# Performance work log

Hardware: AMD Instinct MI355X
Metric: run time of the kernel (lower is better)

## Reference

```python
import jax, jax.numpy as jnp
import numpy as np

INIT_STDEV = 0.01

def setup_inputs() -> dict:
    key = jax.random.key(0)
    k1, k2, k3 = jax.random.split(key, 3)
    B, S, D = 8, 4096, 768
    x = jax.random.normal(k1, (B, S, D), dtype=jnp.float32)
    att_v = jax.random.normal(k2, (D,), dtype=jnp.float32) * INIT_STDEV
    att_W = jax.random.normal(k3, (D, D), dtype=jnp.float32) * INIT_STDEV
    return {"x": x, "att_v": att_v, "att_W": att_W}

def reference(x, att_v, att_W):
    # y = x @ W : [B,S,D]; scores = tanh(y) . v over D : [B,S]
    y = jnp.tanh(jnp.einsum('bsd,de->bse', x, att_W))
    scores = jnp.einsum('bsd,d->bs', y, att_v)
    weights = jax.nn.softmax(scores, axis=-1)            # softmax over sequence
    out = jnp.einsum('bs,bsd->bd', weights, x)           # attsum pool
    return out.astype(jnp.float32)
```

## Files before the change

kernel.cpp:

```cpp
#include <hip/hip_runtime.h>
#include <hip/hip_bf16.h>

constexpr int Bb = 8;
constexpr int Ss = 4096;
constexpr int Dd = 768;
constexpr int Mm = Bb * Ss;

typedef __bf16 bf16x8 __attribute__((ext_vector_type(8)));
typedef __bf16 bf16x4 __attribute__((ext_vector_type(4)));
typedef float f32x4 __attribute__((ext_vector_type(4)));

__device__ __forceinline__ float fast_tanh(float x) {
    return 1.f - 2.f / (__expf(2.f * x) + 1.f);
}

__device__ __forceinline__ void load_lds16(const void* g, void* l) {
    __builtin_amdgcn_global_load_lds(
        (const __attribute__((address_space(1))) unsigned int*)g,
        (__attribute__((address_space(3))) unsigned int*)l, 16, 0, 0);
}

__global__ __launch_bounds__(256) void convWX(const float* __restrict__ W,
                                              __bf16* __restrict__ Wt,
                                              const float* __restrict__ x,
                                              __bf16* __restrict__ xb) {
    const int bid = blockIdx.x;
    if (bid < 576) {
        __shared__ float tile[32][33];
        const int tx = threadIdx.x & 31;
        const int ty = threadIdx.x >> 5;
        const int kb = (bid % 24) * 32;
        const int nb = (bid / 24) * 32;
#pragma unroll
        for (int i = 0; i < 32; i += 8)
            tile[ty + i][tx] = W[(size_t)(kb + ty + i) * Dd + nb + tx];
        __syncthreads();
#pragma unroll
        for (int i = 0; i < 32; i += 8) {
            const int n = nb + ty + i;
            const int txs = (tx & 7) | ((((tx >> 3) & 3) ^ ((n >> 1) & 3)) << 3);
            Wt[(size_t)n * Dd + kb + txs] = (__bf16)tile[tx][ty + i];
        }
    } else {
        const size_t i = ((size_t)(bid - 576) * 256 + threadIdx.x) * 8;
        const int m = (int)(i / Dd);
        const int k = (int)(i % Dd);
        const int sl = (k >> 3) & 3;
        const int dk = (k & ~31) | (((sl ^ ((m >> 1) & 3)) << 3));
        const float4 a = *(const float4*)(x + i);
        const float4 b = *(const float4*)(x + i + 4);
        bf16x8 p;
        p[0] = (__bf16)a.x; p[1] = (__bf16)a.y; p[2] = (__bf16)a.z; p[3] = (__bf16)a.w;
        p[4] = (__bf16)b.x; p[5] = (__bf16)b.y; p[6] = (__bf16)b.z; p[7] = (__bf16)b.w;
        *(bf16x8*)(xb + (size_t)m * Dd + dk) = p;
    }
}

__global__ __launch_bounds__(512, 4) void scores_gemm(
    const __bf16* __restrict__ xb, const __bf16* __restrict__ Wt,
    const float* __restrict__ v, float* __restrict__ scores3) {
    __shared__ __bf16 As[3][128 * 32];
    __shared__ __bf16 Bs[3][256 * 32];
    __shared__ float ssc[8][64];

    const int t = threadIdx.x;
    const int id = blockIdx.x;
    const int ids = ((id & 7) * 96) + (id >> 3);
    const int mb = ids / 3;
    const int nb = ids - mb * 3;
    const int lane = t & 63;
    const int wave = t >> 6;
    const int wm = wave >> 2;
    const int wn = wave & 3;
    const int quad = lane >> 4;
    const int lid = lane & 15;
    const int rslot = ((quad ^ ((lid >> 1) & 3)) * 8);

    const __bf16* axg = xb + (size_t)(mb * 128 + (t >> 2)) * Dd + (t & 3) * 8;
    const int awl = t * 8;

    const __bf16* bgp[2];
    int blp[2];
#pragma unroll
    for (int j = 0; j < 2; ++j) {
        const int flat = j * 8192 + t * 16;
        const int col = flat >> 6;
        bgp[j] = Wt + (size_t)(nb * 256 + col) * Dd + ((flat & 63) >> 1);
        blp[j] = flat >> 1;
    }

    f32x4 acc[4][4];
#pragma unroll
    for (int tm = 0; tm < 4; ++tm)
#pragma unroll
        for (int nt = 0; nt < 4; ++nt) acc[tm][nt] = (f32x4){0.f, 0.f, 0.f, 0.f};

    load_lds16(axg, &As[0][awl]);
#pragma unroll
    for (int j = 0; j < 2; ++j) load_lds16(bgp[j], &Bs[0][blp[j]]);
    load_lds16(axg + 32, &As[1][awl]);
#pragma unroll
    for (int j = 0; j < 2; ++j) load_lds16(bgp[j] + 32, &Bs[1][blp[j]]);

#pragma unroll
    for (int k = 0; k < 24; ++k) {
        if (k == 23) asm volatile("s_waitcnt vmcnt(0)" ::: "memory");
        else         asm volatile("s_waitcnt vmcnt(3)" ::: "memory");
        __builtin_amdgcn_sched_barrier(0);
        __builtin_amdgcn_s_barrier();
        __builtin_amdgcn_sched_barrier(0);

        if (k < 22) {
            load_lds16(axg + (k + 2) * 32, &As[(k + 2) % 3][awl]);
#pragma unroll
            for (int j = 0; j < 2; ++j)
                load_lds16(bgp[j] + (k + 2) * 32, &Bs[(k + 2) % 3][blp[j]]);
        }
        __builtin_amdgcn_sched_barrier(0);

        bf16x8 af[4], bfr[4];
#pragma unroll
        for (int tm = 0; tm < 4; ++tm)
            af[tm] = *(const bf16x8*)(&As[k % 3][(wm * 64 + tm * 16 + lid) * 32 + rslot]);
#pragma unroll
        for (int nt = 0; nt < 4; ++nt)
            bfr[nt] = *(const bf16x8*)(&Bs[k % 3][(wn * 64 + nt * 16 + lid) * 32 + rslot]);

        __builtin_amdgcn_s_setprio(1);
#pragma unroll
        for (int tm = 0; tm < 4; ++tm)
#pragma unroll
            for (int nt = 0; nt < 4; ++nt)
                acc[tm][nt] = __builtin_amdgcn_mfma_f32_16x16x32_bf16(af[tm], bfr[nt], acc[tm][nt], 0, 0, 0);
        __builtin_amdgcn_s_setprio(0);
    }

    float vv[4];
#pragma unroll
    for (int nt = 0; nt < 4; ++nt)
        vv[nt] = v[nb * 256 + wn * 64 + nt * 16 + lid];

#pragma unroll
    for (int tm = 0; tm < 4; ++tm)
#pragma unroll
        for (int r = 0; r < 4; ++r) {
            float s = 0.f;
#pragma unroll
            for (int nt = 0; nt < 4; ++nt) s += vv[nt] * fast_tanh(acc[tm][nt][r]);
            s += __shfl_xor(s, 1);
            s += __shfl_xor(s, 2);
            s += __shfl_xor(s, 4);
            s += __shfl_xor(s, 8);
            if (lid == 0) ssc[wave][tm * 16 + quad * 4 + r] = s;
        }
    __syncthreads();
    if (t < 128) {
        const int wmh = t >> 6;
        const int rl = t & 63;
        float s = 0.f;
#pragma unroll
        for (int ww = 0; ww < 4; ++ww) s += ssc[wmh * 4 + ww][rl];
        scores3[(size_t)nb * Mm + mb * 128 + t] = s;
    }
}

__global__ __launch_bounds__(192) void pool1e(const __bf16* __restrict__ xb,
                                              const float* __restrict__ scores3,
                                              float* __restrict__ partial,
                                              float* __restrict__ esum) {
    const int b = blockIdx.y;
    const int c = blockIdx.x;
    const int t = threadIdx.x;
    __shared__ float we[32];

    if (t < 32) {
        const size_t i = (size_t)b * Ss + c * 32 + t;
        we[t] = __expf(scores3[i] + scores3[Mm + i] + scores3[2 * Mm + i]);
    }
    __syncthreads();

    const int d0 = t * 4;
    const int kc = d0 & ~31;
    const int sl = (d0 >> 3) & 3;
    const int w8 = d0 & 7;
    const int m0 = b * Ss + c * 32;
    const __bf16* base = xb + (size_t)m0 * Dd;

    float4 acc = make_float4(0.f, 0.f, 0.f, 0.f);
#pragma unroll 8
    for (int i = 0; i < 32; ++i) {
        const float ww = we[i];
        const int phys = kc + ((sl ^ (((m0 + i) >> 1) & 3)) << 3) + w8;
        const bf16x4 xv = *(const bf16x4*)(base + (size_t)i * Dd + phys);
        acc.x += ww * (float)xv[0];
        acc.y += ww * (float)xv[1];
        acc.z += ww * (float)xv[2];
        acc.w += ww * (float)xv[3];
    }
    *(float4*)(partial + ((size_t)(b * 128 + c)) * Dd + d0) = acc;
    if (t == 0) {
        float s = 0.f;
#pragma unroll
        for (int i = 0; i < 32; ++i) s += we[i];
        esum[b * 128 + c] = s;
    }
}

__global__ __launch_bounds__(128) void pool2(const float* __restrict__ partial,
                                             const float* __restrict__ esum,
                                             float* __restrict__ out) {
    const int b = blockIdx.y;
    const int t = threadIdx.x;
    const int d = blockIdx.x * 128 + t;

    float es = 0.f;
    if (t < 64) {
        es = esum[b * 128 + t] + esum[b * 128 + 64 + t];
        es += __shfl_xor(es, 1);
        es += __shfl_xor(es, 2);
        es += __shfl_xor(es, 4);
        es += __shfl_xor(es, 8);
        es += __shfl_xor(es, 16);
        es += __shfl_xor(es, 32);
    }
    __shared__ float esT;
    if (t == 0) esT = es;
    __syncthreads();
    const float inv = 1.f / esT;

    float s = 0.f;
#pragma unroll 8
    for (int c = 0; c < 128; ++c) s += partial[((size_t)(b * 128 + c)) * Dd + d];
    out[(size_t)b * Dd + d] = s * inv;
}

extern "C" void kernel_launch(void* const* d_in, const int* in_sizes, int n_in,
                              void* d_out, int out_size, void* d_ws, size_t ws_size,
                              hipStream_t stream) {
    (void)in_sizes; (void)n_in; (void)ws_size; (void)out_size;
    const float* x = (const float*)d_in[0];
    const float* v = (const float*)d_in[1];
    const float* W = (const float*)d_in[2];

    char* ws = (char*)d_ws;
    constexpr size_t OFF_WT = 0;
    constexpr size_t OFF_SC = 1179648;
    constexpr size_t OFF_ES = OFF_SC + 393216;
    constexpr size_t OFF_PA = OFF_ES + 4096;
    constexpr size_t OFF_XB = OFF_PA + 3145728;

    __bf16* Wt     = (__bf16*)(ws + OFF_WT);
    float* scores3 = (float*)(ws + OFF_SC);
    float* esum    = (float*)(ws + OFF_ES);
    float* partial = (float*)(ws + OFF_PA);
    __bf16* xb     = (__bf16*)(ws + OFF_XB);

    convWX<<<dim3(576 + (Mm * Dd) / (256 * 8)), 256, 0, stream>>>(W, Wt, x, xb);
    scores_gemm<<<dim3(3 * Mm / 128), 512, 0, stream>>>(xb, Wt, v, scores3);
    pool1e<<<dim3(128, Bb), 192, 0, stream>>>(xb, scores3, partial, esum);
    pool2<<<dim3(6, Bb), 128, 0, stream>>>(partial, esum, (float*)d_out);
}
```

Before: 219.9 us.

## Shrink GEMM tile to 128x128 with 256 threads and six N-partitions

Changes the scores GEMM block tile from 128x256 (512 threads, 8 waves) to 128x128 (256 threads, 4 waves). The grid doubles, the partial score buffer grows from three to six slices, and the pooling kernel sums six partials. The smaller tile cuts LDS per block and adds more blocks, which may improve occupancy and load balance across CUs. In exchange, x is reloaded from global memory twice as often and more partial scores have to be written and read back.

```diff
diff --git a/kernel.cpp b/kernel.cpp
--- a/kernel.cpp
+++ b/kernel.cpp
@@ -56,37 +56,35 @@
     }
 }
 
-__global__ __launch_bounds__(512, 4) void scores_gemm(
+__global__ __launch_bounds__(256, 3) void scores_gemm(
     const __bf16* __restrict__ xb, const __bf16* __restrict__ Wt,
-    const float* __restrict__ v, float* __restrict__ scores3) {
+    const float* __restrict__ v, float* __restrict__ scores6) {
     __shared__ __bf16 As[3][128 * 32];
-    __shared__ __bf16 Bs[3][256 * 32];
-    __shared__ float ssc[8][64];
+    __shared__ __bf16 Bs[3][128 * 32];
+    __shared__ float ssc[4][64];
 
     const int t = threadIdx.x;
     const int id = blockIdx.x;
-    const int ids = ((id & 7) * 96) + (id >> 3);
-    const int mb = ids / 3;
-    const int nb = ids - mb * 3;
+    const int ids = ((id & 7) * 192) + (id >> 3);
+    const int mb = ids / 6;
+    const int nb = ids - mb * 6;
     const int lane = t & 63;
     const int wave = t >> 6;
-    const int wm = wave >> 2;
-    const int wn = wave & 3;
+    const int wm = wave >> 1;
+    const int wn = wave & 1;
     const int quad = lane >> 4;
     const int lid = lane & 15;
     const int rslot = ((quad ^ ((lid >> 1) & 3)) * 8);
 
-    const __bf16* axg = xb + (size_t)(mb * 128 + (t >> 2)) * Dd + (t & 3) * 8;
-    const int awl = t * 8;
-
+    const __bf16* axg[2];
     const __bf16* bgp[2];
-    int blp[2];
+    int sl_[2];
 #pragma unroll
     for (int j = 0; j < 2; ++j) {
-        const int flat = j * 8192 + t * 16;
-        const int col = flat >> 6;
-        bgp[j] = Wt + (size_t)(nb * 256 + col) * Dd + ((flat & 63) >> 1);
-        blp[j] = flat >> 1;
+        const int row = j * 64 + (t >> 2);
+        axg[j] = xb + (size_t)(mb * 128 + row) * Dd + (t & 3) * 8;
+        bgp[j] = Wt + (size_t)(nb * 128 + row) * Dd + (t & 3) * 8;
+        sl_[j] = j * 2048 + t * 8;
     }
 
     f32x4 acc[4][4];
@@ -95,26 +93,30 @@
 #pragma unroll
         for (int nt = 0; nt < 4; ++nt) acc[tm][nt] = (f32x4){0.f, 0.f, 0.f, 0.f};
 
-    load_lds16(axg, &As[0][awl]);
-#pragma unroll
-    for (int j = 0; j < 2; ++j) load_lds16(bgp[j], &Bs[0][blp[j]]);
-    load_lds16(axg + 32, &As[1][awl]);
-#pragma unroll
-    for (int j = 0; j < 2; ++j) load_lds16(bgp[j] + 32, &Bs[1][blp[j]]);
+#pragma unroll
+    for (int j = 0; j < 2; ++j) load_lds16(axg[j], &As[0][sl_[j]]);
+#pragma unroll
+    for (int j = 0; j < 2; ++j) load_lds16(bgp[j], &Bs[0][sl_[j]]);
+#pragma unroll
+    for (int j = 0; j < 2; ++j) load_lds16(axg[j] + 32, &As[1][sl_[j]]);
+#pragma unroll
+    for (int j = 0; j < 2; ++j) load_lds16(bgp[j] + 32, &Bs[1][sl_[j]]);
 
 #pragma unroll
     for (int k = 0; k < 24; ++k) {
         if (k == 23) asm volatile("s_waitcnt vmcnt(0)" ::: "memory");
-        else         asm volatile("s_waitcnt vmcnt(3)" ::: "memory");
+        else         asm volatile("s_waitcnt vmcnt(4)" ::: "memory");
         __builtin_amdgcn_sched_barrier(0);
         __builtin_amdgcn_s_barrier();
         __builtin_amdgcn_sched_barrier(0);
 
         if (k < 22) {
-            load_lds16(axg + (k + 2) * 32, &As[(k + 2) % 3][awl]);
 #pragma unroll
             for (int j = 0; j < 2; ++j)
-                load_lds16(bgp[j] + (k + 2) * 32, &Bs[(k + 2) % 3][blp[j]]);
+                load_lds16(axg[j] + (k + 2) * 32, &As[(k + 2) % 3][sl_[j]]);
+#pragma unroll
+            for (int j = 0; j < 2; ++j)
+                load_lds16(bgp[j] + (k + 2) * 32, &Bs[(k + 2) % 3][sl_[j]]);
         }
         __builtin_amdgcn_sched_barrier(0);
 
@@ -138,7 +140,7 @@
     float vv[4];
 #pragma unroll
     for (int nt = 0; nt < 4; ++nt)
-        vv[nt] = v[nb * 256 + wn * 64 + nt * 16 + lid];
+        vv[nt] = v[nb * 128 + wn * 64 + nt * 16 + lid];
 
 #pragma unroll
     for (int tm = 0; tm < 4; ++tm)
@@ -157,15 +159,13 @@
     if (t < 128) {
         const int wmh = t >> 6;
         const int rl = t & 63;
-        float s = 0.f;
-#pragma unroll
-        for (int ww = 0; ww < 4; ++ww) s += ssc[wmh * 4 + ww][rl];
-        scores3[(size_t)nb * Mm + mb * 128 + t] = s;
+        const float s = ssc[wmh * 2 + 0][rl] + ssc[wmh * 2 + 1][rl];
+        scores6[(size_t)nb * Mm + mb * 128 + t] = s;
     }
 }
 
 __global__ __launch_bounds__(192) void pool1e(const __bf16* __restrict__ xb,
-                                              const float* __restrict__ scores3,
+                                              const float* __restrict__ scores6,
                                               float* __restrict__ partial,
                                               float* __restrict__ esum) {
     const int b = blockIdx.y;
@@ -175,7 +175,10 @@
 
     if (t < 32) {
         const size_t i = (size_t)b * Ss + c * 32 + t;
-        we[t] = __expf(scores3[i] + scores3[Mm + i] + scores3[2 * Mm + i]);
+        float sc = 0.f;
+#pragma unroll
+        for (int j = 0; j < 6; ++j) sc += scores6[i + (size_t)j * Mm];
+        we[t] = __expf(sc);
     }
     __syncthreads();
 
@@ -245,18 +248,18 @@
     char* ws = (char*)d_ws;
     constexpr size_t OFF_WT = 0;
     constexpr size_t OFF_SC = 1179648;
-    constexpr size_t OFF_ES = OFF_SC + 393216;
+    constexpr size_t OFF_ES = OFF_SC + 786432;
     constexpr size_t OFF_PA = OFF_ES + 4096;
     constexpr size_t OFF_XB = OFF_PA + 3145728;
 
     __bf16* Wt     = (__bf16*)(ws + OFF_WT);
-    float* scores3 = (float*)(ws + OFF_SC);
+    float* scores6 = (float*)(ws + OFF_SC);
     float* esum    = (float*)(ws + OFF_ES);
     float* partial = (float*)(ws + OFF_PA);
     __bf16* xb     = (__bf16*)(ws + OFF_XB);
 
     convWX<<<dim3(576 + (Mm * Dd) / (256 * 8)), 256, 0, stream>>>(W, Wt, x, xb);
-    scores_gemm<<<dim3(3 * Mm / 128), 512, 0, stream>>>(xb, Wt, v, scores3);
-    pool1e<<<dim3(128, Bb), 192, 0, stream>>>(xb, scores3, partial, esum);
+    scores_gemm<<<dim3(6 * Mm / 128), 256, 0, stream>>>(xb, Wt, v, scores6);
+    pool1e<<<dim3(128, Bb), 192, 0, stream>>>(xb, scores6, partial, esum);
     pool2<<<dim3(6, Bb), 128, 0, stream>>>(partial, esum, (float*)d_out);
 }
```

Result: no change. 223.4 us (+1.6%).
